# Kernel optimization log

Hardware: AMD Instinct MI355X
Metric: run time of the kernel (lower is better)

Reference implementation:

```python
import math
import jax, jax.numpy as jnp
import numpy as np

BS, C, HH, HW = 32, 64, 128, 128   # x is NCHW; C == dim
S0, S1 = 2, 2                      # patch size
DIM = 64
K = 512                            # num_embeddings


def setup_inputs() -> dict:
    key = jax.random.key(0)
    k1, k2 = jax.random.split(key)
    x = jax.random.normal(k1, (BS, C, HH, HW), dtype=jnp.float32)
    embed = jax.random.normal(k2, (S0, S1, DIM, K), dtype=jnp.float32) * 0.02
    return {"x": x, "embed": embed}


def reference(x, embed):
    # eval-mode forward (not training): sample = one_hot(argmax(probs))
    bs, Cc, hH, hW = x.shape
    rH, rW = hH // S0, hW // S1
    xp = jnp.transpose(x, (0, 2, 3, 1))                          # [b, hH, hW, C]
    xb = xp.reshape(bs, rH, S0, rW, S1, Cc)
    xb = jnp.transpose(xb, (0, 1, 3, 2, 4, 5))                   # [b, rH, rW, s0, s1, C]
    flat = xb.reshape(-1, S0 * S1 * Cc)                          # [T, D]
    E = embed.reshape(-1, K)                                     # [D, K]
    # squared-distance via matmul
    distances = (jnp.sum(flat * flat, axis=1, keepdims=True)
                 - 2.0 * (flat @ E)
                 + jnp.sum(E * E, axis=0, keepdims=True))        # [T, K]
    logits = jax.nn.log_softmax(-distances, axis=-1)             # dist.logits (normalized)
    probs = jnp.exp(logits)                                      # dist.probs
    embed_ind_flat = jnp.argmax(probs, axis=-1)                  # [T]
    sample = jax.nn.one_hot(embed_ind_flat, K, dtype=flat.dtype) # [T, K]
    embed_ind = embed_ind_flat.reshape(bs, rH, rW)
    quantize = jnp.einsum('tk,hwdk->thwd', sample, embed)        # [T, s0, s1, dim]
    quantize = quantize.reshape(bs, rH, rW, S0, S1, Cc)
    quantize = jnp.transpose(quantize, (0, 1, 3, 2, 4, 5)).reshape(bs, hH, hW, Cc)
    quantize = jnp.transpose(quantize, (0, 3, 1, 2))             # [b, C, hH, hW]
    KL = jnp.where(probs == 0, 0.0, probs * (logits + math.log(K)))
    diff = KL.sum() / bs * (32 * 32 * 3.0)
    diff = diff * 0.0
    avg_probs = jnp.mean(sample, axis=1)                         # [T] (faithful: mean over K)
    perplexity = jnp.exp(-jnp.sum(avg_probs * jnp.log(avg_probs + 1e-10), axis=-1))
    return quantize, diff, embed_ind, perplexity
```

## Files before the change

kernel.cpp:

```cpp
#include <hip/hip_runtime.h>


#define OFF_DIFF    33554432
#define OFF_IND     33554433
#define OFF_PERP    33685505

typedef __attribute__((ext_vector_type(8))) short short8;
typedef __attribute__((ext_vector_type(4))) float f32x4;

__device__ __forceinline__ unsigned short f2bf(float f) {
    unsigned int u = __float_as_uint(f);
    return (unsigned short)((u + 0x7FFFu + ((u >> 16) & 1u)) >> 16);
}
__device__ __forceinline__ float bf2f(unsigned short h) {
    return __uint_as_float(((unsigned int)h) << 16);
}

__device__ __forceinline__ void gload_lds16(const void* g, void* l) {
    __builtin_amdgcn_global_load_lds(
        (const __attribute__((address_space(1))) unsigned int*)g,
        (__attribute__((address_space(3))) unsigned int*)l, 16, 0, 0);
}

__global__ void vq_split(const float* __restrict__ E,
                         float* __restrict__ Et,
                         short* __restrict__ EhiSw,
                         short* __restrict__ EloSw,
                         float* __restrict__ ssqe,
                         float* __restrict__ out) {
    const int k = blockIdx.x;
    const int t = threadIdx.x;
    float v[4];
    #pragma unroll
    for (int j = 0; j < 4; ++j) v[j] = E[(t * 4 + j) * 512 + k];
    *(float4*)&Et[k * 256 + t * 4] = make_float4(v[0], v[1], v[2], v[3]);

    unsigned short h[4], l[4];
    #pragma unroll
    for (int j = 0; j < 4; ++j) {
        h[j] = f2bf(v[j]);
        l[j] = f2bf(v[j] - bf2f(h[j]));
    }
    uint2 H = make_uint2((unsigned)h[0] | ((unsigned)h[1] << 16),
                         (unsigned)h[2] | ((unsigned)h[3] << 16));
    uint2 L = make_uint2((unsigned)l[0] | ((unsigned)l[1] << 16),
                         (unsigned)l[2] | ((unsigned)l[3] << 16));
    int pos = k * 256 + 8 * ((t >> 1) ^ (k & 7)) + (t & 1) * 4;
    *(uint2*)&EhiSw[pos] = H;
    *(uint2*)&EloSw[pos] = L;

    float s = fmaf(v[0], v[0], fmaf(v[1], v[1], fmaf(v[2], v[2], v[3] * v[3])));
    #pragma unroll
    for (int m = 1; m < 64; m <<= 1) s += __shfl_xor(s, m, 64);
    if (t == 0) {
        ssqe[k] = s;
        if (k == 0) {
            out[OFF_DIFF] = 0.0f;
            out[OFF_PERP] = 0.0f;
        }
    }
}

__device__ __forceinline__ void stage4(short* Th, short* Tl, int tok, int dbase,
                                       float a, float b, float c, float d) {
    int idx = tok * 256 + (dbase ^ ((tok & 7) << 3));
    unsigned short h0 = f2bf(a), h1 = f2bf(b), h2 = f2bf(c), h3 = f2bf(d);
    *(uint2*)&Th[idx] = make_uint2((unsigned)h0 | ((unsigned)h1 << 16),
                                   (unsigned)h2 | ((unsigned)h3 << 16));
    unsigned short l0 = f2bf(a - bf2f(h0)), l1 = f2bf(b - bf2f(h1));
    unsigned short l2 = f2bf(c - bf2f(h2)), l3 = f2bf(d - bf2f(h3));
    *(uint2*)&Tl[idx] = make_uint2((unsigned)l0 | ((unsigned)l1 << 16),
                                   (unsigned)l2 | ((unsigned)l3 << 16));
}

#define MFMA(A, B, C) __builtin_amdgcn_mfma_f32_16x16x32_bf16(A, B, C, 0, 0, 0)

__global__ __launch_bounds__(256, 2)
void vq_main_mfma(const float* __restrict__ x,
                  const float* __restrict__ Et,
                  const short* __restrict__ EhiSw,
                  const short* __restrict__ EloSw,
                  const float* __restrict__ ssqe,
                  float* __restrict__ out) {
    __shared__ __attribute__((aligned(16))) unsigned char smem[68352];
    short* Thi = (short*)smem;
    short* Tlo = (short*)(smem + 32768);
    float* Q   = (float*)smem;
    float* ssqe_sh = (float*)(smem + 65792);
    int*   kstar   = (int*)(smem + 67840);

    const int g   = blockIdx.x;
    const int b   = g >> 5;
    const int rh2 = g & 31;
    const int tid = threadIdx.x;
    const int wv  = tid >> 6;
    const int ln  = tid & 63;
    const int r   = ln & 15;
    const int tq  = ln >> 4;

    ssqe_sh[tid]       = ssqe[tid];
    ssqe_sh[tid + 256] = ssqe[tid + 256];

    short8 Bh0[8], Bl0[8], Bh1[8], Bl1[8];
    const int tokr = wv * 16 + r;

    {
        const float* xrow = x + (size_t)b * 1048576 + (size_t)(rh2 * 2) * 256;
        #pragma unroll
        for (int i = 0; i < 4; ++i) {
            int j    = tid + i * 256;
            int col4 = j & 31;
            int rest = j >> 5;
            int c4   = rest & 15;
            int s0   = rest >> 4;
            const float* p = xrow + (c4 * 4) * 16384 + s0 * 128 + col4 * 4;
            float4 v0 = *(const float4*)(p);
            float4 v1 = *(const float4*)(p + 16384);
            float4 v2 = *(const float4*)(p + 32768);
            float4 v3 = *(const float4*)(p + 49152);
            int tokA = col4 * 2, tokB = tokA + 1;
            int d0 = s0 * 128 + c4 * 4, d1 = d0 + 64;
            stage4(Thi, Tlo, tokA, d0, v0.x, v1.x, v2.x, v3.x);
            stage4(Thi, Tlo, tokA, d1, v0.y, v1.y, v2.y, v3.y);
            stage4(Thi, Tlo, tokB, d0, v0.z, v1.z, v2.z, v3.z);
            stage4(Thi, Tlo, tokB, d1, v0.w, v1.w, v2.w, v3.w);
        }
        __syncthreads();
        #pragma unroll
        for (int ks = 0; ks < 8; ++ks) {
            int idx = tokr * 256 + ((ks * 32 + tq * 8) ^ ((tokr & 7) << 3));
            Bh0[ks] = *(const short8*)&Thi[idx];
            Bl0[ks] = *(const short8*)&Tlo[idx];
        }
        __syncthreads();
    }
    {
        const float* xrow = x + (size_t)b * 1048576 + (size_t)(rh2 * 2 + 1) * 256;
        #pragma unroll
        for (int i = 0; i < 4; ++i) {
            int j    = tid + i * 256;
            int col4 = j & 31;
            int rest = j >> 5;
            int c4   = rest & 15;
            int s0   = rest >> 4;
            const float* p = xrow + (c4 * 4) * 16384 + s0 * 128 + col4 * 4;
            float4 v0 = *(const float4*)(p);
            float4 v1 = *(const float4*)(p + 16384);
            float4 v2 = *(const float4*)(p + 32768);
            float4 v3 = *(const float4*)(p + 49152);
            int tokA = col4 * 2, tokB = tokA + 1;
            int d0 = s0 * 128 + c4 * 4, d1 = d0 + 64;
            stage4(Thi, Tlo, tokA, d0, v0.x, v1.x, v2.x, v3.x);
            stage4(Thi, Tlo, tokA, d1, v0.y, v1.y, v2.y, v3.y);
            stage4(Thi, Tlo, tokB, d0, v0.z, v1.z, v2.z, v3.z);
            stage4(Thi, Tlo, tokB, d1, v0.w, v1.w, v2.w, v3.w);
        }
        __syncthreads();
        #pragma unroll
        for (int ks = 0; ks < 8; ++ks) {
            int idx = tokr * 256 + ((ks * 32 + tq * 8) ^ ((tokr & 7) << 3));
            Bh1[ks] = *(const short8*)&Thi[idx];
            Bl1[ks] = *(const short8*)&Tlo[idx];
        }
        __syncthreads();
    }

    {
        const char* hs = (const char*)EhiSw;
        const char* ls = (const char*)EloSw;
        char* d = (char*)smem;
        int o = wv * 1024 + ln * 16;
        gload_lds16(hs + o,        d + wv * 1024);
        gload_lds16(hs + o + 4096, d + wv * 1024 + 4096);
        gload_lds16(ls + o,        d + wv * 1024 + 8192);
        gload_lds16(ls + o + 4096, d + wv * 1024 + 12288);
    }
    __syncthreads();

    float best0 = __builtin_inff(), best1 = __builtin_inff();
    int   bi0 = 0, bi1 = 0;
    int   cur = 0;

    for (int ct = 0; ct < 32; ++ct) {
        if (ct < 31) {
            const char* hs = (const char*)EhiSw + (ct + 1) * 8192;
            const char* ls = (const char*)EloSw + (ct + 1) * 8192;
            char* d = (char*)smem + (cur ^ 1) * 16384;
            int o = wv * 1024 + ln * 16;
            gload_lds16(hs + o,        d + wv * 1024);
            gload_lds16(hs + o + 4096, d + wv * 1024 + 4096);
            gload_lds16(ls + o,        d + wv * 1024 + 8192);
            gload_lds16(ls + o + 4096, d + wv * 1024 + 12288);
        }
        const short* bh = (const short*)(smem + cur * 16384);
        const short* bl = bh + 4096;
        f32x4 acc0 = {0.f, 0.f, 0.f, 0.f};
        f32x4 acc1 = {0.f, 0.f, 0.f, 0.f};
        #pragma unroll
        for (int ks = 0; ks < 8; ++ks) {
            int off = r * 256 + 8 * (((ks * 4 + tq)) ^ (r & 7));
            short8 ah = *(const short8*)&bh[off];
            short8 al = *(const short8*)&bl[off];
            acc0 = MFMA(ah, Bh0[ks], acc0);
            acc1 = MFMA(ah, Bh1[ks], acc1);
            acc0 = MFMA(ah, Bl0[ks], acc0);
            acc1 = MFMA(ah, Bl1[ks], acc1);
            acc0 = MFMA(al, Bh0[ks], acc0);
            acc1 = MFMA(al, Bh1[ks], acc1);
        }
        float4 sq = *(const float4*)&ssqe_sh[ct * 16 + tq * 4];
        int kb = ct * 16 + tq * 4;
        {
            float s0v = fmaf(-2.0f, acc0[0], sq.x);
            float s1v = fmaf(-2.0f, acc0[1], sq.y);
            float s2v = fmaf(-2.0f, acc0[2], sq.z);
            float s3v = fmaf(-2.0f, acc0[3], sq.w);
            if (s0v < best0) { best0 = s0v; bi0 = kb;     }
            if (s1v < best0) { best0 = s1v; bi0 = kb + 1; }
            if (s2v < best0) { best0 = s2v; bi0 = kb + 2; }
            if (s3v < best0) { best0 = s3v; bi0 = kb + 3; }
        }
        {
            float s0v = fmaf(-2.0f, acc1[0], sq.x);
            float s1v = fmaf(-2.0f, acc1[1], sq.y);
            float s2v = fmaf(-2.0f, acc1[2], sq.z);
            float s3v = fmaf(-2.0f, acc1[3], sq.w);
            if (s0v < best1) { best1 = s0v; bi1 = kb;     }
            if (s1v < best1) { best1 = s1v; bi1 = kb + 1; }
            if (s2v < best1) { best1 = s2v; bi1 = kb + 2; }
            if (s3v < best1) { best1 = s3v; bi1 = kb + 3; }
        }
        __syncthreads();
        cur ^= 1;
    }

    #pragma unroll
    for (int m = 16; m <= 32; m <<= 1) {
        float ob = __shfl_xor(best0, m, 64);
        int   oi = __shfl_xor(bi0, m, 64);
        if (ob < best0 || (ob == best0 && oi < bi0)) { best0 = ob; bi0 = oi; }
        float pb = __shfl_xor(best1, m, 64);
        int   pi = __shfl_xor(bi1, m, 64);
        if (pb < best1 || (pb == best1 && pi < bi1)) { best1 = pb; bi1 = pi; }
    }
    if (tq == 0) {
        kstar[tokr]      = bi0;
        kstar[64 + tokr] = bi1;
        size_t ib = (size_t)OFF_IND + (size_t)b * 4096 + (size_t)(rh2 * 2) * 64;
        out[ib + tokr]      = (float)bi0;
        out[ib + 64 + tokr] = (float)bi1;
    }
    __syncthreads();

    #pragma unroll
    for (int rr = 0; rr < 2; ++rr) {
        if (rr) __syncthreads();
        {
            int qtok = tid & 63, part = tid >> 6;
            const float* Erow = Et + (size_t)kstar[rr * 64 + qtok] * 256 + part * 64;
            float* qrow = Q + qtok * 257 + part * 64;
            #pragma unroll
            for (int u = 0; u < 16; ++u) {
                float4 vv = *(const float4*)(Erow + u * 4);
                qrow[u * 4]     = vv.x;
                qrow[u * 4 + 1] = vv.y;
                qrow[u * 4 + 2] = vv.z;
                qrow[u * 4 + 3] = vv.w;
            }
        }
        __syncthreads();
        float* ob2 = out + (size_t)b * 1048576 + (size_t)(rh2 * 2 + rr) * 256;
        #pragma unroll
        for (int i = 0; i < 16; ++i) {
            int j    = tid + i * 256;
            int row  = j >> 5;
            int col4 = j & 31;
            int c  = row >> 1;
            int s0 = row & 1;
            int tokA = col4 * 2, tokB = tokA + 1;
            int d0 = s0 * 128 + c, d1 = d0 + 64;
            float4 v;
            v.x = Q[tokA * 257 + d0];
            v.y = Q[tokA * 257 + d1];
            v.z = Q[tokB * 257 + d0];
            v.w = Q[tokB * 257 + d1];
            *(float4*)(ob2 + c * 16384 + s0 * 128 + col4 * 4) = v;
        }
    }
}

__global__ void vq_prep(const float* __restrict__ E,
                        float* __restrict__ ssqe,
                        float* __restrict__ out) {
    int k = blockIdx.x * 256 + threadIdx.x;
    float acc = 0.0f;
    #pragma unroll 8
    for (int d = 0; d < 256; ++d) {
        float e = E[d * 512 + k];
        acc = fmaf(e, e, acc);
    }
    ssqe[k] = acc;
    if (k == 0) { out[OFF_DIFF] = 0.0f; out[OFF_PERP] = 0.0f; }
}

__global__ __launch_bounds__(256, 2)
void vq_main_f32(const float* __restrict__ x,
                 const float* __restrict__ E,
                 const float* __restrict__ ssqe,
                 float* __restrict__ out) {
    __shared__ float A[256 * 64];
    __shared__ float redD[4][64];
    __shared__ int   redI[4][64];
    __shared__ int   kstar_sh[64];

    const int g = blockIdx.x, b = g >> 6, rh = g & 63, tid = threadIdx.x;
    const float* xbase = x + (size_t)b * 1048576 + rh * 256;

    #pragma unroll
    for (int i = 0; i < 16; ++i) {
        int j = tid + i * 256;
        int row = j >> 5, col4 = j & 31;
        int c = row >> 1, s0 = row & 1;
        const float4 v = *(const float4*)(xbase + c * 16384 + s0 * 128 + col4 * 4);
        int tokk = col4 * 2;
        int d0 = s0 * 128 + c, d1 = d0 + 64;
        *(float2*)&A[d0 * 64 + tokk] = make_float2(v.x, v.z);
        *(float2*)&A[d1 * 64 + tokk] = make_float2(v.y, v.w);
    }
    __syncthreads();

    const int wave = tid >> 6, lane = tid & 63;
    float ssq = 0.0f;
    #pragma unroll 8
    for (int d = 0; d < 256; ++d) { float a = A[d * 64 + lane]; ssq = fmaf(a, a, ssq); }

    const int K0 = __builtin_amdgcn_readfirstlane(wave * 128);
    float best = __builtin_inff();
    int besti = 0;
    for (int chunk = 0; chunk < 8; ++chunk) {
        const int k0 = K0 + chunk * 16;
        const float* __restrict__ Ep = E + k0;
        float acc[16];
        #pragma unroll
        for (int j = 0; j < 16; ++j) acc[j] = 0.0f;
        #pragma unroll 4
        for (int d = 0; d < 256; ++d) {
            float a = A[d * 64 + lane];
            #pragma unroll
            for (int j = 0; j < 16; ++j) acc[j] = fmaf(a, Ep[d * 512 + j], acc[j]);
        }
        #pragma unroll
        for (int j = 0; j < 16; ++j) {
            float dist = (ssq - 2.0f * acc[j]) + ssqe[k0 + j];
            if (dist < best) { best = dist; besti = k0 + j; }
        }
    }
    redD[wave][lane] = best; redI[wave][lane] = besti;
    __syncthreads();
    if (tid < 64) {
        float bd = redD[0][tid]; int bi = redI[0][tid];
        #pragma unroll
        for (int w = 1; w < 4; ++w) {
            float dd = redD[w][tid];
            if (dd < bd) { bd = dd; bi = redI[w][tid]; }
        }
        kstar_sh[tid] = bi;
        out[OFF_IND + g * 64 + tid] = (float)bi;
    }
    __syncthreads();
    float* obase = out + (size_t)b * 1048576 + rh * 256;
    #pragma unroll
    for (int i = 0; i < 16; ++i) {
        int j = tid + i * 256;
        int row = j >> 5, col4 = j & 31;
        int c = row >> 1, s0 = row & 1;
        int tokA = col4 * 2, tokB = tokA + 1;
        int kA = kstar_sh[tokA], kB = kstar_sh[tokB];
        int d0 = s0 * 128 + c, d1 = d0 + 64;
        float4 v;
        v.x = E[d0 * 512 + kA]; v.y = E[d1 * 512 + kA];
        v.z = E[d0 * 512 + kB]; v.w = E[d1 * 512 + kB];
        *(float4*)(obase + c * 16384 + s0 * 128 + col4 * 4) = v;
    }
}

extern "C" void kernel_launch(void* const* d_in, const int* in_sizes, int n_in,
                              void* d_out, int out_size, void* d_ws, size_t ws_size,
                              hipStream_t stream) {
    const float* x = (const float*)d_in[0];
    const float* E = (const float*)d_in[1];
    float* out = (float*)d_out;

    float* ssqe  = (float*)d_ws;
    float* Et    = (float*)((char*)d_ws + 4096);
    short* EhiSw = (short*)((char*)d_ws + 528384);
    short* EloSw = (short*)((char*)d_ws + 790528);
    const size_t need = 1052672;

    if (ws_size >= need) {
        hipLaunchKernelGGL(vq_split, dim3(512), dim3(64), 0, stream,
                           E, Et, EhiSw, EloSw, ssqe, out);
        hipLaunchKernelGGL(vq_main_mfma, dim3(1024), dim3(256), 0, stream,
                           x, Et, EhiSw, EloSw, ssqe, out);
    } else {
        hipLaunchKernelGGL(vq_prep, dim3(2), dim3(256), 0, stream, E, ssqe, out);
        hipLaunchKernelGGL(vq_main_f32, dim3(2048), dim3(256), 0, stream,
                           x, E, ssqe, out);
    }
}
```

Baseline: 306.2 us.

## Halve tokens per block to raise occupancy and split MFMA accumulation chains

Each block now handles one 64-token patch row instead of two, which halves the LDS footprint and the register-resident token fragments, and launches twice as many blocks with a higher launch-bounds occupancy target. The staging layout uses a new XOR swizzle over 32 local tokens. The inner MFMA loop splits accumulation into even and odd chains to shorten dependency latency. In exchange, every block re-streams the entire codebook from global/L2, so codebook traffic per token doubles.

```diff
diff --git a/kernel.cpp b/kernel.cpp
--- a/kernel.cpp
+++ b/kernel.cpp
@@ -61,9 +61,10 @@
     }
 }
 
-__device__ __forceinline__ void stage4(short* Th, short* Tl, int tok, int dbase,
+__device__ __forceinline__ void stage4(short* Th, short* Tl, int lt, int f,
+                                       int dbase,
                                        float a, float b, float c, float d) {
-    int idx = tok * 256 + (dbase ^ ((tok & 7) << 3));
+    int idx = lt * 256 + (dbase ^ (f << 3));
     unsigned short h0 = f2bf(a), h1 = f2bf(b), h2 = f2bf(c), h3 = f2bf(d);
     *(uint2*)&Th[idx] = make_uint2((unsigned)h0 | ((unsigned)h1 << 16),
                                    (unsigned)h2 | ((unsigned)h3 << 16));
@@ -74,93 +75,70 @@
 }
 
 #define MFMA(A, B, C) __builtin_amdgcn_mfma_f32_16x16x32_bf16(A, B, C, 0, 0, 0)
-
-__global__ __launch_bounds__(256, 2)
+#define FSWZ(lt) ((((lt) >> 1) ^ ((lt) >> 4)) & 7)
+
+__global__ __launch_bounds__(256, 4)
 void vq_main_mfma(const float* __restrict__ x,
                   const float* __restrict__ Et,
                   const short* __restrict__ EhiSw,
                   const short* __restrict__ EloSw,
                   const float* __restrict__ ssqe,
                   float* __restrict__ out) {
-    __shared__ __attribute__((aligned(16))) unsigned char smem[68352];
+    __shared__ __attribute__((aligned(16))) unsigned char smem[35328];
     short* Thi = (short*)smem;
-    short* Tlo = (short*)(smem + 32768);
+    short* Tlo = (short*)(smem + 16384);
     float* Q   = (float*)smem;
-    float* ssqe_sh = (float*)(smem + 65792);
-    int*   kstar   = (int*)(smem + 67840);
+    float* ssqe_sh = (float*)(smem + 33024);
+    int*   kstar   = (int*)(smem + 35072);
 
     const int g   = blockIdx.x;
-    const int b   = g >> 5;
-    const int rh2 = g & 31;
+    const int b   = g >> 6;
+    const int rh  = g & 63;
     const int tid = threadIdx.x;
     const int wv  = tid >> 6;
     const int ln  = tid & 63;
     const int r   = ln & 15;
     const int tq  = ln >> 4;
+    const int tokr = wv * 16 + r;
 
     ssqe_sh[tid]       = ssqe[tid];
     ssqe_sh[tid + 256] = ssqe[tid + 256];
 
-    short8 Bh0[8], Bl0[8], Bh1[8], Bl1[8];
-    const int tokr = wv * 16 + r;
-
-    {
-        const float* xrow = x + (size_t)b * 1048576 + (size_t)(rh2 * 2) * 256;
-        #pragma unroll
-        for (int i = 0; i < 4; ++i) {
-            int j    = tid + i * 256;
-            int col4 = j & 31;
-            int rest = j >> 5;
-            int c4   = rest & 15;
-            int s0   = rest >> 4;
-            const float* p = xrow + (c4 * 4) * 16384 + s0 * 128 + col4 * 4;
+    short8 Bh[8], Bl[8];
+    const float* xrow = x + (size_t)b * 1048576 + (size_t)rh * 256;
+
+    #pragma unroll
+    for (int hp = 0; hp < 2; ++hp) {
+        #pragma unroll
+        for (int i = 0; i < 2; ++i) {
+            int j     = tid + i * 256;
+            int col4h = j & 15;
+            int rest  = j >> 4;
+            int c4    = rest & 15;
+            int s0    = rest >> 4;
+            const float* p = xrow + (c4 * 4) * 16384 + s0 * 128 + hp * 64 + col4h * 4;
             float4 v0 = *(const float4*)(p);
             float4 v1 = *(const float4*)(p + 16384);
             float4 v2 = *(const float4*)(p + 32768);
             float4 v3 = *(const float4*)(p + 49152);
-            int tokA = col4 * 2, tokB = tokA + 1;
+            int ltA = col4h * 2, ltB = ltA + 1;
+            int fA = FSWZ(ltA), fB = FSWZ(ltB);
             int d0 = s0 * 128 + c4 * 4, d1 = d0 + 64;
-            stage4(Thi, Tlo, tokA, d0, v0.x, v1.x, v2.x, v3.x);
-            stage4(Thi, Tlo, tokA, d1, v0.y, v1.y, v2.y, v3.y);
-            stage4(Thi, Tlo, tokB, d0, v0.z, v1.z, v2.z, v3.z);
-            stage4(Thi, Tlo, tokB, d1, v0.w, v1.w, v2.w, v3.w);
+            stage4(Thi, Tlo, ltA, fA, d0, v0.x, v1.x, v2.x, v3.x);
+            stage4(Thi, Tlo, ltA, fA, d1, v0.y, v1.y, v2.y, v3.y);
+            stage4(Thi, Tlo, ltB, fB, d0, v0.z, v1.z, v2.z, v3.z);
+            stage4(Thi, Tlo, ltB, fB, d1, v0.w, v1.w, v2.w, v3.w);
         }
         __syncthreads();
-        #pragma unroll
-        for (int ks = 0; ks < 8; ++ks) {
-            int idx = tokr * 256 + ((ks * 32 + tq * 8) ^ ((tokr & 7) << 3));
-            Bh0[ks] = *(const short8*)&Thi[idx];
-            Bl0[ks] = *(const short8*)&Tlo[idx];
-        }
-        __syncthreads();
-    }
-    {
-        const float* xrow = x + (size_t)b * 1048576 + (size_t)(rh2 * 2 + 1) * 256;
-        #pragma unroll
-        for (int i = 0; i < 4; ++i) {
-            int j    = tid + i * 256;
-            int col4 = j & 31;
-            int rest = j >> 5;
-            int c4   = rest & 15;
-            int s0   = rest >> 4;
-            const float* p = xrow + (c4 * 4) * 16384 + s0 * 128 + col4 * 4;
-            float4 v0 = *(const float4*)(p);
-            float4 v1 = *(const float4*)(p + 16384);
-            float4 v2 = *(const float4*)(p + 32768);
-            float4 v3 = *(const float4*)(p + 49152);
-            int tokA = col4 * 2, tokB = tokA + 1;
-            int d0 = s0 * 128 + c4 * 4, d1 = d0 + 64;
-            stage4(Thi, Tlo, tokA, d0, v0.x, v1.x, v2.x, v3.x);
-            stage4(Thi, Tlo, tokA, d1, v0.y, v1.y, v2.y, v3.y);
-            stage4(Thi, Tlo, tokB, d0, v0.z, v1.z, v2.z, v3.z);
-            stage4(Thi, Tlo, tokB, d1, v0.w, v1.w, v2.w, v3.w);
-        }
-        __syncthreads();
-        #pragma unroll
-        for (int ks = 0; ks < 8; ++ks) {
-            int idx = tokr * 256 + ((ks * 32 + tq * 8) ^ ((tokr & 7) << 3));
-            Bh1[ks] = *(const short8*)&Thi[idx];
-            Bl1[ks] = *(const short8*)&Tlo[idx];
+        if ((tokr >> 5) == hp) {
+            int lt = tokr & 31;
+            int f  = FSWZ(lt);
+            #pragma unroll
+            for (int ks = 0; ks < 8; ++ks) {
+                int idx = lt * 256 + ((ks * 32 + tq * 8) ^ (f << 3));
+                Bh[ks] = *(const short8*)&Thi[idx];
+                Bl[ks] = *(const short8*)&Tlo[idx];
+            }
         }
         __syncthreads();
     }
@@ -177,9 +155,9 @@
     }
     __syncthreads();
 
-    float best0 = __builtin_inff(), best1 = __builtin_inff();
-    int   bi0 = 0, bi1 = 0;
-    int   cur = 0;
+    float best  = __builtin_inff();
+    int   besti = 0;
+    int   cur   = 0;
 
     for (int ct = 0; ct < 32; ++ct) {
         if (ct < 31) {
@@ -194,73 +172,58 @@
         }
         const short* bh = (const short*)(smem + cur * 16384);
         const short* bl = bh + 4096;
-        f32x4 acc0 = {0.f, 0.f, 0.f, 0.f};
-        f32x4 acc1 = {0.f, 0.f, 0.f, 0.f};
-        #pragma unroll
-        for (int ks = 0; ks < 8; ++ks) {
-            int off = r * 256 + 8 * (((ks * 4 + tq)) ^ (r & 7));
-            short8 ah = *(const short8*)&bh[off];
-            short8 al = *(const short8*)&bl[off];
-            acc0 = MFMA(ah, Bh0[ks], acc0);
-            acc1 = MFMA(ah, Bh1[ks], acc1);
-            acc0 = MFMA(ah, Bl0[ks], acc0);
-            acc1 = MFMA(ah, Bl1[ks], acc1);
-            acc0 = MFMA(al, Bh0[ks], acc0);
-            acc1 = MFMA(al, Bh1[ks], acc1);
+        f32x4 ae = {0.f, 0.f, 0.f, 0.f};
+        f32x4 ao = {0.f, 0.f, 0.f, 0.f};
+        #pragma unroll
+        for (int ks = 0; ks < 8; ks += 2) {
+            int off0 = r * 256 + 8 * ((ks * 4 + tq) ^ (r & 7));
+            short8 ah0 = *(const short8*)&bh[off0];
+            short8 al0 = *(const short8*)&bl[off0];
+            int off1 = r * 256 + 8 * (((ks + 1) * 4 + tq) ^ (r & 7));
+            short8 ah1 = *(const short8*)&bh[off1];
+            short8 al1 = *(const short8*)&bl[off1];
+            ae = MFMA(ah0, Bh[ks], ae);
+            ao = MFMA(ah1, Bh[ks + 1], ao);
+            ae = MFMA(ah0, Bl[ks], ae);
+            ao = MFMA(ah1, Bl[ks + 1], ao);
+            ae = MFMA(al0, Bh[ks], ae);
+            ao = MFMA(al1, Bh[ks + 1], ao);
         }
         float4 sq = *(const float4*)&ssqe_sh[ct * 16 + tq * 4];
         int kb = ct * 16 + tq * 4;
-        {
-            float s0v = fmaf(-2.0f, acc0[0], sq.x);
-            float s1v = fmaf(-2.0f, acc0[1], sq.y);
-            float s2v = fmaf(-2.0f, acc0[2], sq.z);
-            float s3v = fmaf(-2.0f, acc0[3], sq.w);
-            if (s0v < best0) { best0 = s0v; bi0 = kb;     }
-            if (s1v < best0) { best0 = s1v; bi0 = kb + 1; }
-            if (s2v < best0) { best0 = s2v; bi0 = kb + 2; }
-            if (s3v < best0) { best0 = s3v; bi0 = kb + 3; }
-        }
-        {
-            float s0v = fmaf(-2.0f, acc1[0], sq.x);
-            float s1v = fmaf(-2.0f, acc1[1], sq.y);
-            float s2v = fmaf(-2.0f, acc1[2], sq.z);
-            float s3v = fmaf(-2.0f, acc1[3], sq.w);
-            if (s0v < best1) { best1 = s0v; bi1 = kb;     }
-            if (s1v < best1) { best1 = s1v; bi1 = kb + 1; }
-            if (s2v < best1) { best1 = s2v; bi1 = kb + 2; }
-            if (s3v < best1) { best1 = s3v; bi1 = kb + 3; }
-        }
+        float s0v = fmaf(-2.0f, ae[0] + ao[0], sq.x);
+        float s1v = fmaf(-2.0f, ae[1] + ao[1], sq.y);
+        float s2v = fmaf(-2.0f, ae[2] + ao[2], sq.z);
+        float s3v = fmaf(-2.0f, ae[3] + ao[3], sq.w);
+        if (s0v < best) { best = s0v; besti = kb;     }
+        if (s1v < best) { best = s1v; besti = kb + 1; }
+        if (s2v < best) { best = s2v; besti = kb + 2; }
+        if (s3v < best) { best = s3v; besti = kb + 3; }
         __syncthreads();
         cur ^= 1;
     }
 
     #pragma unroll
     for (int m = 16; m <= 32; m <<= 1) {
-        float ob = __shfl_xor(best0, m, 64);
-        int   oi = __shfl_xor(bi0, m, 64);
-        if (ob < best0 || (ob == best0 && oi < bi0)) { best0 = ob; bi0 = oi; }
-        float pb = __shfl_xor(best1, m, 64);
-        int   pi = __shfl_xor(bi1, m, 64);
-        if (pb < best1 || (pb == best1 && pi < bi1)) { best1 = pb; bi1 = pi; }
+        float ob = __shfl_xor(best, m, 64);
+        int   oi = __shfl_xor(besti, m, 64);
+        if (ob < best || (ob == best && oi < besti)) { best = ob; besti = oi; }
     }
     if (tq == 0) {
-        kstar[tokr]      = bi0;
-        kstar[64 + tokr] = bi1;
-        size_t ib = (size_t)OFF_IND + (size_t)b * 4096 + (size_t)(rh2 * 2) * 64;
-        out[ib + tokr]      = (float)bi0;
-        out[ib + 64 + tokr] = (float)bi1;
-    }
-    __syncthreads();
-
-    #pragma unroll
-    for (int rr = 0; rr < 2; ++rr) {
-        if (rr) __syncthreads();
+        kstar[tokr] = besti;
+        out[OFF_IND + (size_t)g * 64 + tokr] = (float)besti;
+    }
+    __syncthreads();
+
+    #pragma unroll
+    for (int hp = 0; hp < 2; ++hp) {
+        if (hp) __syncthreads();
         {
-            int qtok = tid & 63, part = tid >> 6;
-            const float* Erow = Et + (size_t)kstar[rr * 64 + qtok] * 256 + part * 64;
-            float* qrow = Q + qtok * 257 + part * 64;
+            int qt = tid & 31, part = tid >> 5;
+            const float* Erow = Et + (size_t)kstar[hp * 32 + qt] * 256 + part * 32;
+            float* qrow = Q + qt * 257 + part * 32;
             #pragma unroll
-            for (int u = 0; u < 16; ++u) {
+            for (int u = 0; u < 8; ++u) {
                 float4 vv = *(const float4*)(Erow + u * 4);
                 qrow[u * 4]     = vv.x;
                 qrow[u * 4 + 1] = vv.y;
@@ -269,22 +232,22 @@
             }
         }
         __syncthreads();
-        float* ob2 = out + (size_t)b * 1048576 + (size_t)(rh2 * 2 + rr) * 256;
-        #pragma unroll
-        for (int i = 0; i < 16; ++i) {
-            int j    = tid + i * 256;
-            int row  = j >> 5;
-            int col4 = j & 31;
-            int c  = row >> 1;
-            int s0 = row & 1;
-            int tokA = col4 * 2, tokB = tokA + 1;
+        float* ob2 = out + (size_t)b * 1048576 + rh * 256 + hp * 64;
+        #pragma unroll
+        for (int i = 0; i < 8; ++i) {
+            int j     = tid + i * 256;
+            int col4h = j & 15;
+            int rest  = j >> 4;
+            int c  = rest >> 1;
+            int s0 = rest & 1;
+            int ltA = col4h * 2, ltB = ltA + 1;
             int d0 = s0 * 128 + c, d1 = d0 + 64;
             float4 v;
-            v.x = Q[tokA * 257 + d0];
-            v.y = Q[tokA * 257 + d1];
-            v.z = Q[tokB * 257 + d0];
-            v.w = Q[tokB * 257 + d1];
-            *(float4*)(ob2 + c * 16384 + s0 * 128 + col4 * 4) = v;
+            v.x = Q[ltA * 257 + d0];
+            v.y = Q[ltA * 257 + d1];
+            v.z = Q[ltB * 257 + d0];
+            v.w = Q[ltB * 257 + d1];
+            *(float4*)(ob2 + c * 16384 + s0 * 128 + col4h * 4) = v;
         }
     }
 }
@@ -400,7 +363,7 @@
     if (ws_size >= need) {
         hipLaunchKernelGGL(vq_split, dim3(512), dim3(64), 0, stream,
                            E, Et, EhiSw, EloSw, ssqe, out);
-        hipLaunchKernelGGL(vq_main_mfma, dim3(1024), dim3(256), 0, stream,
+        hipLaunchKernelGGL(vq_main_mfma, dim3(2048), dim3(256), 0, stream,
                            x, Et, EhiSw, EloSw, ssqe, out);
     } else {
         hipLaunchKernelGGL(vq_prep, dim3(2), dim3(256), 0, stream, E, ssqe, out);
```

Result: no change. 305.1 us (-0.4%).
